# Kernel optimization log

Hardware: AMD Instinct MI355X
Metric: run time of the kernel (lower is better)

Reference implementation:

```python
import jax, jax.numpy as jnp
import numpy as np

TOP_K = 2  # config.moe_config['moe_top_k']


def setup_inputs() -> dict:
    key = jax.random.key(0)
    k1, k2, k3, k4 = jax.random.split(key, 4)
    B, S, H, F, E = 2, 1024, 1024, 2048, 8
    def init(k, shape, fan_in):
        return jax.random.normal(k, shape, jnp.float32) / np.float32(np.sqrt(fan_in))
    return {
        "hidden_states": jax.random.normal(k1, (B, S, H), jnp.float32),
        "router_w": init(k2, (H, E), H),          # Linear(hidden, E, bias=False)
        "W1": init(k3, (E, H, 2 * F), H),          # per-expert Linear(hidden, 2*ffn)
        "W2": init(k4, (E, F, H), F),              # per-expert Linear(ffn, hidden)
    }


def reference(hidden_states, router_w, W1, W2):
    B, S, H = hidden_states.shape
    E = router_w.shape[1]
    x = hidden_states.reshape(-1, H)                      # [N, H], N = B*S
    N = x.shape[0]

    # router: logits -> fp32 softmax -> top-k -> renormalize (matches torch)
    logits = x @ router_w                                  # [N, E]
    probs = jax.nn.softmax(logits.astype(jnp.float32), axis=-1)
    rw, sel = jax.lax.top_k(probs, TOP_K)                  # [N, k]
    rw = rw / rw.sum(axis=-1, keepdims=True)
    rw = rw.astype(x.dtype)

    # combine weights per (token, expert); top-k experts are distinct so add==set
    cw = jnp.zeros((N, E), x.dtype).at[jnp.arange(N)[:, None], sel].add(rw)

    # per-expert SwiGLU MLP over all tokens, masked combine (full-capacity MoE)
    h = jnp.einsum('nh,ehf->enf', x, W1)                   # [E, N, 2F]
    a, b = jnp.split(h, 2, axis=-1)                        # gate, value halves
    g = jax.nn.silu(a) * b                                 # [E, N, F]
    y = jnp.einsum('enf,efh->enh', g, W2)                  # [E, N, H]
    out = jnp.einsum('enh,ne->nh', y, cw)                  # weighted scatter-combine
    return out.reshape(B, S, H)
```

## Files before the change

### kernel.cpp

```cpp
#include <hip/hip_runtime.h>
#include <hip/hip_bf16.h>

#define H_DIM 1024
#define E_NUM 8
#define F_DIM 2048
#define N_TOK 2048
typedef unsigned int uint;
typedef short bf16x8 __attribute__((ext_vector_type(8)));
typedef float f32x4 __attribute__((ext_vector_type(4)));

#define WS_CNT   0
#define WS_LIST  256
#define WS_W     (WS_LIST + 8*N_TOK*4)
#define WS_G     131072
#define WS_Y     (WS_G + 4096*2048*2)
#define WS_XB    WS_Y


static __device__ __forceinline__ uint f2bf(float f) {
    uint u = __builtin_bit_cast(uint, f);
    return (u + 0x7FFFu + ((u >> 16) & 1u)) >> 16;
}
static __device__ __forceinline__ float bflo(uint u) { return __builtin_bit_cast(float, u << 16); }
static __device__ __forceinline__ float bfhi(uint u) { return __builtin_bit_cast(float, u & 0xFFFF0000u); }
static __device__ __forceinline__ uint cvtpk(float a, float b) {
    uint r;
    asm("v_cvt_pk_bf16_f32 %0, %1, %2" : "=v"(r) : "v"(a), "v"(b));
    return r;
}
static __device__ __forceinline__ void gload_lds16(const void* g, void* l) {
    __builtin_amdgcn_global_load_lds(
        (const __attribute__((address_space(1))) unsigned int*)g,
        (__attribute__((address_space(3))) unsigned int*)l,
        16, 0, 0);
}
template<int N> static __device__ __forceinline__ void vmwait() {
    if constexpr (N == 0)      asm volatile("s_waitcnt vmcnt(0)" ::: "memory");
    else if constexpr (N == 4) asm volatile("s_waitcnt vmcnt(4)" ::: "memory");
    else if constexpr (N == 5) asm volatile("s_waitcnt vmcnt(5)" ::: "memory");
    else if constexpr (N == 6) asm volatile("s_waitcnt vmcnt(6)" ::: "memory");
}

__global__ __launch_bounds__(256) void cvt_x_kernel(const float* __restrict__ x,
                                                    unsigned short* __restrict__ xb)
{
    int c = blockIdx.x * 256 + threadIdx.x;
    int row = c >> 7, b = c & 127;
    int t = b >> 3, s = b & 7;
    int klo = t*64 + (s >> 2)*32 + (s & 3)*4;
    const float* xr = x + (size_t)row * H_DIM;
    float4 lo = *(const float4*)(xr + klo);
    float4 hi = *(const float4*)(xr + klo + 16);
    uint4 o;
    o.x = cvtpk(lo.x, lo.y); o.y = cvtpk(lo.z, lo.w);
    o.z = cvtpk(hi.x, hi.y); o.w = cvtpk(hi.z, hi.w);
    *(uint4*)(xb + (size_t)row * H_DIM + b*8) = o;
}

__global__ __launch_bounds__(256) void router_kernel(
    const float* __restrict__ x, const float* __restrict__ rw,
    int* __restrict__ cnt, int* __restrict__ list, float* __restrict__ w_entry)
{
    int wave = threadIdx.x >> 6, lane = threadIdx.x & 63;
    int n = blockIdx.x * 4 + wave;
    const float* xr = x + (size_t)n * H_DIM;
    float acc[8] = {0,0,0,0,0,0,0,0};
    #pragma unroll
    for (int i = 0; i < H_DIM/64; ++i) {
        int h = i*64 + lane;
        float xv = xr[h];
        const float4* rr = (const float4*)(rw + (size_t)h*8);
        float4 r0 = rr[0], r1 = rr[1];
        acc[0] += xv*r0.x; acc[1] += xv*r0.y; acc[2] += xv*r0.z; acc[3] += xv*r0.w;
        acc[4] += xv*r1.x; acc[5] += xv*r1.y; acc[6] += xv*r1.z; acc[7] += xv*r1.w;
    }
    #pragma unroll
    for (int e = 0; e < 8; ++e) {
        float v = acc[e];
        #pragma unroll
        for (int off = 32; off; off >>= 1) v += __shfl_xor(v, off);
        acc[e] = v;
    }
    int e0 = 0;
    #pragma unroll
    for (int e = 1; e < 8; ++e) if (acc[e] > acc[e0]) e0 = e;
    int e1 = -1;
    #pragma unroll
    for (int e = 0; e < 8; ++e) if (e != e0 && (e1 < 0 || acc[e] > acc[e1])) e1 = e;
    float w0 = 1.0f / (1.0f + __expf(acc[e1] - acc[e0]));
    float w1 = 1.0f - w0;
    if (lane == 0) {
        int p0 = atomicAdd(&cnt[e0], 1);
        list[e0*N_TOK + p0] = n*2;
        w_entry[n*2] = w0;
        int p1 = atomicAdd(&cnt[e1], 1);
        list[e1*N_TOK + p1] = n*2 + 1;
        w_entry[n*2+1] = w1;
    }
}

template<int IS_G1>
__global__ __launch_bounds__(256, IS_G1 ? 3 : 4) void moe_gemm_kernel(
    const unsigned short* __restrict__ Asrc, const float* __restrict__ W,
    const int* __restrict__ cnt, const int* __restrict__ list,
    const float* __restrict__ w_entry, unsigned short* __restrict__ dst)
{
    constexpr int KTOT  = IS_G1 ? H_DIM : F_DIM;
    constexpr int BLD   = IS_G1 ? 2*F_DIM : H_DIM;
    constexpr int DLD   = IS_G1 ? F_DIM : H_DIM;
    constexpr int ALD   = IS_G1 ? H_DIM : F_DIM;
    constexpr int ROWS  = IS_G1 ? 64 : 32;
    constexpr int NM    = ROWS / 16;
    constexpr int NA    = ROWS / 32;
    constexpr int NMT   = 2048 / ROWS;
    constexpr int NNT   = IS_G1 ? 32 : 8;
    constexpr int NT    = KTOT / 32;
    constexpr int ODDW  = 4 + NA;

    __shared__ __align__(16) unsigned short As[2][ROWS*64];
    __shared__ __align__(16) uint Bs[2][32*128];

    constexpr int nb = NMT * NNT * E_NUM;
    constexpr int chunk = nb >> 3;
    int bid = blockIdx.x;
    int f  = (bid & 7) * chunk + (bid >> 3);
    int mt = f % NMT;
    int nt = (f / NMT) % NNT;
    int e  = f / (NMT * NNT);

    const int c = cnt[e];
    if (mt * ROWS >= c) return;
    const int tid = threadIdx.x;
    const int lane = tid & 63, wid = tid >> 6;
    const int l15 = lane & 15, lg = lane >> 4;
    const int lbase = e * N_TOK + mt * ROWS;

    const unsigned short* a_src[NA];
    #pragma unroll
    for (int i = 0; i < NA; ++i) {
        int sl  = wid*(NA*1024) + i*1024 + lane*16;
        int row = sl >> 7;
        int kb  = ((sl >> 4) & 7) ^ (row & 7);
        int rr  = (mt*ROWS + row) < c ? row : (c - 1 - mt*ROWS);
        int ent = list[lbase + rr];
        int arow = IS_G1 ? (ent >> 1) : ent;
        a_src[i] = Asrc + (size_t)arow * ALD + kb*8;
    }

    const float* Wb = W + (size_t)e * (size_t)(IS_G1 ? H_DIM*2*F_DIM : F_DIM*H_DIM);
    const float* b_srcp[4];
    #pragma unroll
    for (int i = 0; i < 4; ++i) {
        int k  = wid*8 + i*2 + (lane >> 5);
        int c4 = (lane & 31) ^ (k & 12);
        int gc;
        if constexpr (IS_G1) gc = (c4 < 16) ? (nt*64 + 4*c4) : (F_DIM + nt*64 + 4*(c4-16));
        else                 gc = nt*128 + 4*c4;
        b_srcp[i] = Wb + (size_t)k * BLD + gc;
    }

    int a_addr[NM][2];
    #pragma unroll
    for (int m = 0; m < NM; ++m)
        #pragma unroll
        for (int p = 0; p < 2; ++p) {
            int row = m*16 + l15;
            a_addr[m][p] = row*128 + ((p*64 + lg*16) ^ ((row & 7) << 4));
        }
    int b_base[2];
    #pragma unroll
    for (int j = 0; j < 2; ++j) {
        int cb = IS_G1 ? (j ? (4 + wid) : wid) : (wid*2 + j);
        b_base[j] = ((cb*16 + l15) * 4) ^ (lg << 6);
    }

    f32x4 acc[NM][2];
    #pragma unroll
    for (int m = 0; m < NM; ++m)
        #pragma unroll
        for (int j = 0; j < 2; ++j) acc[m][j] = (f32x4){0.f,0.f,0.f,0.f};

    auto STAGE_A = [&](int s) {
        #pragma unroll
        for (int i = 0; i < NA; ++i)
            gload_lds16(a_src[i] + s*64, (char*)As[s & 1] + wid*(NA*1024) + i*1024);
    };
    auto STAGE_B = [&](int t) {
        #pragma unroll
        for (int i = 0; i < 4; ++i)
            gload_lds16(b_srcp[i] + (size_t)t * 32 * BLD, (char*)Bs[t & 1] + wid*4096 + i*1024);
    };
    auto compute = [&](int P, int abuf) {
        const char* ab  = (const char*)As[abuf];
        const char* bb0 = (const char*)Bs[P];
        bf16x8 af[NM];
        #pragma unroll
        for (int m = 0; m < NM; ++m)
            af[m] = *(const bf16x8*)(ab + (P ? a_addr[m][1] : a_addr[m][0]));
        bf16x8 bfr[2];
        #pragma unroll
        for (int j = 0; j < 2; ++j) {
            const char* bb = bb0 + (4*lg)*512 + b_base[j];
            float fA0 = *(const float*)(bb);
            float fA1 = *(const float*)(bb + 512);
            float fA2 = *(const float*)(bb + 1024);
            float fA3 = *(const float*)(bb + 1536);
            float fB0 = *(const float*)(bb + 8192);
            float fB1 = *(const float*)(bb + 8192 + 512);
            float fB2 = *(const float*)(bb + 8192 + 1024);
            float fB3 = *(const float*)(bb + 8192 + 1536);
            union { uint u[4]; bf16x8 v; } bu;
            bu.u[0] = cvtpk(fA0, fA1);
            bu.u[1] = cvtpk(fA2, fA3);
            bu.u[2] = cvtpk(fB0, fB1);
            bu.u[3] = cvtpk(fB2, fB3);
            bfr[j] = bu.v;
        }
        #pragma unroll
        for (int m = 0; m < NM; ++m)
            #pragma unroll
            for (int j = 0; j < 2; ++j)
                acc[m][j] = __builtin_amdgcn_mfma_f32_16x16x32_bf16(af[m], bfr[j], acc[m][j], 0, 0, 0);
    };

    STAGE_A(0); STAGE_B(0); STAGE_B(1);

    for (int tp = 0; tp < NT/2 - 1; ++tp) {
        const int t = 2*tp, ab = tp & 1;
        vmwait<4>();
        __builtin_amdgcn_sched_barrier(0);
        __builtin_amdgcn_s_barrier();
        asm volatile("" ::: "memory");
        compute(0, ab);
        asm volatile("" ::: "memory");
        __builtin_amdgcn_s_barrier();
        asm volatile("" ::: "memory");
        STAGE_A(tp + 1);
        STAGE_B(t + 2);
        vmwait<ODDW>();
        __builtin_amdgcn_sched_barrier(0);
        __builtin_amdgcn_s_barrier();
        asm volatile("" ::: "memory");
        compute(1, ab);
        asm volatile("" ::: "memory");
        __builtin_amdgcn_s_barrier();
        asm volatile("" ::: "memory");
        STAGE_B(t + 3);
    }
    {
        const int ab = (NT/2 - 1) & 1;
        vmwait<4>();
        __builtin_amdgcn_sched_barrier(0);
        __builtin_amdgcn_s_barrier();
        asm volatile("" ::: "memory");
        compute(0, ab);
        asm volatile("" ::: "memory");
        vmwait<0>();
        __builtin_amdgcn_sched_barrier(0);
        __builtin_amdgcn_s_barrier();
        asm volatile("" ::: "memory");
        compute(1, ab);
    }

    if constexpr (IS_G1) {
        unsigned short (*tb)[64] = (unsigned short (*)[64])As;
        const int pcol = ((wid >> 1)*4 + (l15 >> 2))*8 + (wid & 1)*4 + (l15 & 3);
        #pragma unroll
        for (int m = 0; m < NM; ++m) {
            f32x4 ga = acc[m][0], gv = acc[m][1];
            #pragma unroll
            for (int i = 0; i < 4; ++i) {
                int row = m*16 + lg*4 + i;
                float a = ga[i];
                tb[row][pcol] = (unsigned short)f2bf((a / (1.f + __expf(-a))) * gv[i]);
            }
        }
        __syncthreads();
        int r = tid >> 3, ch = tid & 7;
        #pragma unroll
        for (int h = 0; h < 2; ++h) {
            int rr = r + h*32;
            if (mt*64 + rr < c) {
                int ent = list[lbase + rr];
                uint4 v = *(const uint4*)&tb[rr][ch*8];
                *(uint4*)((char*)dst + ((size_t)ent * DLD + nt*64)*2 + ch*16) = v;
            }
        }
    } else {
        float (*tb)[128] = (float (*)[128])Bs;
        #pragma unroll
        for (int m = 0; m < NM; ++m)
            #pragma unroll
            for (int j = 0; j < 2; ++j)
                #pragma unroll
                for (int i = 0; i < 4; ++i) {
                    int row = m*16 + lg*4 + i;
                    tb[row][(wid*2 + j)*16 + l15] = acc[m][j][i];
                }
        __syncthreads();
        int r = tid >> 3, ch = tid & 7;
        if (mt*32 + r < c) {
            int ent = list[lbase + r];
            float w = w_entry[ent];
            const float* src = &tb[r][ch*16];
            uint4 o0, o1;
            o0.x = cvtpk(w*src[0],  w*src[1]);  o0.y = cvtpk(w*src[2],  w*src[3]);
            o0.z = cvtpk(w*src[4],  w*src[5]);  o0.w = cvtpk(w*src[6],  w*src[7]);
            o1.x = cvtpk(w*src[8],  w*src[9]);  o1.y = cvtpk(w*src[10], w*src[11]);
            o1.z = cvtpk(w*src[12], w*src[13]); o1.w = cvtpk(w*src[14], w*src[15]);
            char* dp = (char*)dst + ((size_t)ent * DLD + nt*128 + ch*16)*2;
            *(uint4*)(dp)      = o0;
            *(uint4*)(dp + 16) = o1;
        }
    }
}

__global__ __launch_bounds__(256) void combine_kernel(
    const unsigned short* __restrict__ y, float* __restrict__ out)
{
    int gid = blockIdx.x * 256 + threadIdx.x;
    size_t base = (size_t)gid * 8;
    int n = (int)(base >> 10), h = (int)(base & 1023);
    const uint4 a = *(const uint4*)(y + (size_t)(2*n)   * 1024 + h);
    const uint4 b = *(const uint4*)(y + (size_t)(2*n+1) * 1024 + h);
    float4 o0, o1;
    o0.x = bflo(a.x)+bflo(b.x); o0.y = bfhi(a.x)+bfhi(b.x);
    o0.z = bflo(a.y)+bflo(b.y); o0.w = bfhi(a.y)+bfhi(b.y);
    o1.x = bflo(a.z)+bflo(b.z); o1.y = bfhi(a.z)+bfhi(b.z);
    o1.z = bflo(a.w)+bflo(b.w); o1.w = bfhi(a.w)+bfhi(b.w);
    *(float4*)(out + base)     = o0;
    *(float4*)(out + base + 4) = o1;
}

extern "C" void kernel_launch(void* const* d_in, const int* in_sizes, int n_in,
                              void* d_out, int out_size, void* d_ws, size_t ws_size,
                              hipStream_t stream) {
    const float* x  = (const float*)d_in[0];
    const float* rw = (const float*)d_in[1];
    const float* W1 = (const float*)d_in[2];
    const float* W2 = (const float*)d_in[3];
    float* out = (float*)d_out;
    char* ws = (char*)d_ws;
    int*   cnt     = (int*)(ws + WS_CNT);
    int*   list    = (int*)(ws + WS_LIST);
    float* w_entry = (float*)(ws + WS_W);
    unsigned short* g  = (unsigned short*)(ws + WS_G);
    unsigned short* y  = (unsigned short*)(ws + WS_Y);
    unsigned short* xb = (unsigned short*)(ws + WS_XB);

    hipMemsetAsync(cnt, 0, E_NUM * sizeof(int), stream);
    cvt_x_kernel<<<N_TOK*H_DIM/2048, 256, 0, stream>>>(x, xb);
    router_kernel<<<N_TOK/4, 256, 0, stream>>>(x, rw, cnt, list, w_entry);
    moe_gemm_kernel<1><<<32*32*E_NUM, 256, 0, stream>>>(xb, W1, cnt, list, w_entry, g);
    moe_gemm_kernel<0><<<64*8*E_NUM, 256, 0, stream>>>(g,  W2, cnt, list, w_entry, y);
    combine_kernel<<<(out_size/8 + 255)/256, 256, 0, stream>>>(y, out);
}
```

Before: 237.4 us.

## Enlarge MoE GEMM row tile to 128 tokens with chunked epilogues

Both expert GEMMs now process 128 token rows per block instead of 64 (gate/up) or 32 (down). Each fp32 weight tile is therefore loaded and converted fewer times per expert. To fit, occupancy is lowered to 2 blocks per CU, and A fragments are loaded one at a time inside the MFMA loop to limit register pressure. The epilogues are rewritten: the down-projection writes back in four 32-row chunks through the shared buffer, and a barrier is added before the gate/up epilogue reuses the A buffer. The trade-off is fewer blocks, lower occupancy and more padding waste on partially filled expert tiles.

Measured after the change: 225.9 us. 1.05x faster.

```diff
diff --git a/kernel.cpp b/kernel.cpp
--- a/kernel.cpp
+++ b/kernel.cpp
@@ -37,8 +37,7 @@
 template<int N> static __device__ __forceinline__ void vmwait() {
     if constexpr (N == 0)      asm volatile("s_waitcnt vmcnt(0)" ::: "memory");
     else if constexpr (N == 4) asm volatile("s_waitcnt vmcnt(4)" ::: "memory");
-    else if constexpr (N == 5) asm volatile("s_waitcnt vmcnt(5)" ::: "memory");
-    else if constexpr (N == 6) asm volatile("s_waitcnt vmcnt(6)" ::: "memory");
+    else if constexpr (N == 8) asm volatile("s_waitcnt vmcnt(8)" ::: "memory");
 }
 
 __global__ __launch_bounds__(256) void cvt_x_kernel(const float* __restrict__ x,
@@ -100,7 +99,7 @@
 }
 
 template<int IS_G1>
-__global__ __launch_bounds__(256, IS_G1 ? 3 : 4) void moe_gemm_kernel(
+__global__ __launch_bounds__(256, 2) void moe_gemm_kernel(
     const unsigned short* __restrict__ Asrc, const float* __restrict__ W,
     const int* __restrict__ cnt, const int* __restrict__ list,
     const float* __restrict__ w_entry, unsigned short* __restrict__ dst)
@@ -109,13 +108,12 @@
     constexpr int BLD   = IS_G1 ? 2*F_DIM : H_DIM;
     constexpr int DLD   = IS_G1 ? F_DIM : H_DIM;
     constexpr int ALD   = IS_G1 ? H_DIM : F_DIM;
-    constexpr int ROWS  = IS_G1 ? 64 : 32;
-    constexpr int NM    = ROWS / 16;
-    constexpr int NA    = ROWS / 32;
-    constexpr int NMT   = 2048 / ROWS;
+    constexpr int ROWS  = 128;
+    constexpr int NM    = 8;
+    constexpr int NA    = 4;
+    constexpr int NMT   = 16;
     constexpr int NNT   = IS_G1 ? 32 : 8;
     constexpr int NT    = KTOT / 32;
-    constexpr int ODDW  = 4 + NA;
 
     __shared__ __align__(16) unsigned short As[2][ROWS*64];
     __shared__ __align__(16) uint Bs[2][32*128];
@@ -193,10 +191,6 @@
     auto compute = [&](int P, int abuf) {
         const char* ab  = (const char*)As[abuf];
         const char* bb0 = (const char*)Bs[P];
-        bf16x8 af[NM];
-        #pragma unroll
-        for (int m = 0; m < NM; ++m)
-            af[m] = *(const bf16x8*)(ab + (P ? a_addr[m][1] : a_addr[m][0]));
         bf16x8 bfr[2];
         #pragma unroll
         for (int j = 0; j < 2; ++j) {
@@ -217,10 +211,12 @@
             bfr[j] = bu.v;
         }
         #pragma unroll
-        for (int m = 0; m < NM; ++m)
+        for (int m = 0; m < NM; ++m) {
+            bf16x8 af = *(const bf16x8*)(ab + (P ? a_addr[m][1] : a_addr[m][0]));
             #pragma unroll
             for (int j = 0; j < 2; ++j)
-                acc[m][j] = __builtin_amdgcn_mfma_f32_16x16x32_bf16(af[m], bfr[j], acc[m][j], 0, 0, 0);
+                acc[m][j] = __builtin_amdgcn_mfma_f32_16x16x32_bf16(af, bfr[j], acc[m][j], 0, 0, 0);
+        }
     };
 
     STAGE_A(0); STAGE_B(0); STAGE_B(1);
@@ -237,7 +233,7 @@
         asm volatile("" ::: "memory");
         STAGE_A(tp + 1);
         STAGE_B(t + 2);
-        vmwait<ODDW>();
+        vmwait<8>();
         __builtin_amdgcn_sched_barrier(0);
         __builtin_amdgcn_s_barrier();
         asm volatile("" ::: "memory");
@@ -263,6 +259,7 @@
     }
 
     if constexpr (IS_G1) {
+        __syncthreads();
         unsigned short (*tb)[64] = (unsigned short (*)[64])As;
         const int pcol = ((wid >> 1)*4 + (l15 >> 2))*8 + (wid & 1)*4 + (l15 & 3);
         #pragma unroll
@@ -276,41 +273,47 @@
             }
         }
         __syncthreads();
-        int r = tid >> 3, ch = tid & 7;
-        #pragma unroll
-        for (int h = 0; h < 2; ++h) {
-            int rr = r + h*32;
-            if (mt*64 + rr < c) {
-                int ent = list[lbase + rr];
-                uint4 v = *(const uint4*)&tb[rr][ch*8];
-                *(uint4*)((char*)dst + ((size_t)ent * DLD + nt*64)*2 + ch*16) = v;
-            }
+        int r = tid >> 1, half = tid & 1;
+        if (mt*ROWS + r < c) {
+            int ent = list[lbase + r];
+            char* dp = (char*)dst + ((size_t)ent * DLD + nt*64)*2 + half*64;
+            const char* sp = (const char*)&tb[r][0] + half*64;
+            #pragma unroll
+            for (int q = 0; q < 4; ++q)
+                *(uint4*)(dp + q*16) = *(const uint4*)(sp + q*16);
         }
     } else {
         float (*tb)[128] = (float (*)[128])Bs;
         #pragma unroll
-        for (int m = 0; m < NM; ++m)
+        for (int h = 0; h < 4; ++h) {
+            __syncthreads();
             #pragma unroll
-            for (int j = 0; j < 2; ++j)
+            for (int mm = 0; mm < 2; ++mm) {
+                int m = h*2 + mm;
                 #pragma unroll
-                for (int i = 0; i < 4; ++i) {
-                    int row = m*16 + lg*4 + i;
-                    tb[row][(wid*2 + j)*16 + l15] = acc[m][j][i];
-                }
-        __syncthreads();
-        int r = tid >> 3, ch = tid & 7;
-        if (mt*32 + r < c) {
-            int ent = list[lbase + r];
-            float w = w_entry[ent];
-            const float* src = &tb[r][ch*16];
-            uint4 o0, o1;
-            o0.x = cvtpk(w*src[0],  w*src[1]);  o0.y = cvtpk(w*src[2],  w*src[3]);
-            o0.z = cvtpk(w*src[4],  w*src[5]);  o0.w = cvtpk(w*src[6],  w*src[7]);
-            o1.x = cvtpk(w*src[8],  w*src[9]);  o1.y = cvtpk(w*src[10], w*src[11]);
-            o1.z = cvtpk(w*src[12], w*src[13]); o1.w = cvtpk(w*src[14], w*src[15]);
-            char* dp = (char*)dst + ((size_t)ent * DLD + nt*128 + ch*16)*2;
-            *(uint4*)(dp)      = o0;
-            *(uint4*)(dp + 16) = o1;
+                for (int j = 0; j < 2; ++j)
+                    #pragma unroll
+                    for (int i = 0; i < 4; ++i) {
+                        int row = mm*16 + lg*4 + i;
+                        tb[row][(wid*2 + j)*16 + l15] = acc[m][j][i];
+                    }
+            }
+            __syncthreads();
+            int r = tid >> 3, ch = tid & 7;
+            int rg = h*32 + r;
+            if (mt*ROWS + rg < c) {
+                int ent = list[lbase + rg];
+                float w = w_entry[ent];
+                const float* src = &tb[r][ch*16];
+                uint4 o0, o1;
+                o0.x = cvtpk(w*src[0],  w*src[1]);  o0.y = cvtpk(w*src[2],  w*src[3]);
+                o0.z = cvtpk(w*src[4],  w*src[5]);  o0.w = cvtpk(w*src[6],  w*src[7]);
+                o1.x = cvtpk(w*src[8],  w*src[9]);  o1.y = cvtpk(w*src[10], w*src[11]);
+                o1.z = cvtpk(w*src[12], w*src[13]); o1.w = cvtpk(w*src[14], w*src[15]);
+                char* dp = (char*)dst + ((size_t)ent * DLD + nt*128 + ch*16)*2;
+                *(uint4*)(dp)      = o0;
+                *(uint4*)(dp + 16) = o1;
+            }
         }
     }
 }
@@ -351,7 +354,7 @@
     hipMemsetAsync(cnt, 0, E_NUM * sizeof(int), stream);
     cvt_x_kernel<<<N_TOK*H_DIM/2048, 256, 0, stream>>>(x, xb);
     router_kernel<<<N_TOK/4, 256, 0, stream>>>(x, rw, cnt, list, w_entry);
-    moe_gemm_kernel<1><<<32*32*E_NUM, 256, 0, stream>>>(xb, W1, cnt, list, w_entry, g);
-    moe_gemm_kernel<0><<<64*8*E_NUM, 256, 0, stream>>>(g,  W2, cnt, list, w_entry, y);
+    moe_gemm_kernel<1><<<16*32*E_NUM, 256, 0, stream>>>(xb, W1, cnt, list, w_entry, g);
+    moe_gemm_kernel<0><<<16*8*E_NUM, 256, 0, stream>>>(g,  W2, cnt, list, w_entry, y);
     combine_kernel<<<(out_size/8 + 255)/256, 256, 0, stream>>>(y, out);
 }
```
